# Kernel optimization log

Measured on AMD Instinct MI355X. Metric: run time of the kernel, lower is better.

## Reference

```python
import jax, jax.numpy as jnp
import numpy as np

B, H, N = 2, 4, 8192
K = 32       # sub_size
TEMP = 2.0   # temperature for the soft permutation indicator


def setup_inputs() -> dict:
    key = jax.random.key(0)
    ranking = jax.random.normal(key, (B, H, N, 1), dtype=jnp.float32)
    return {"ranking": ranking, "i": 0, "j": N}


@jax.custom_vjp
def hsigmoid(x):
    # Hard step indicator (x > 0) with straight-through gradient (CoCN Hsigmoid)
    return (x > 0).astype(x.dtype)

def _hs_fwd(x):
    return hsigmoid(x), None

def _hs_bwd(res, g):
    return (g,)

hsigmoid.defvjp(_hs_fwd, _hs_bwd)


def _windows(x, n, k):
    # circular pad last dim by k-1, then unfold into sliding windows of size k
    xp = jnp.concatenate([x, x[..., :k - 1]], axis=-1)
    idx = jnp.arange(n)[:, None] + jnp.arange(k)[None, :]   # (n, k)
    return xp[..., idx]                                      # (..., n, k)


def reference(ranking, i, j):
    b, h, n = ranking.shape[:3]
    k = K
    r = ranking[..., 0]                                      # (b,h,n)
    order = jnp.argsort(r, axis=2, stable=True)              # (b,h,n) stable sort indices
    r_sorted = jnp.take_along_axis(r, order, axis=2)

    val_win = _windows(r_sorted, n, k)                       # (b,h,n,k)
    idx_win = _windows(order.astype(jnp.float32), n, k).astype(jnp.int32)

    # scatter windows back to original node order == gather by inverse permutation
    inv = jnp.argsort(order, axis=2)                         # (b,h,n)
    val_win = jnp.take_along_axis(val_win, inv[..., None], axis=2)
    idx_win = jnp.take_along_axis(idx_win, inv[..., None], axis=2)

    # within each window, sort by original node index (stable), reorder values alike
    k_order = jnp.argsort(idx_win, axis=-1, stable=True)
    sorted_idx = jnp.take_along_axis(idx_win, k_order, axis=-1)
    val_win = jnp.take_along_axis(val_win, k_order, axis=-1)

    # slice node window [i, i+j)
    val_win = val_win[:, :, i:i + j]                         # (b,h,j,k)
    sorted_idx = sorted_idx[:, :, i:i + j]

    # (b,j,h,k) -> (b*j, h, k, 1)
    x = jnp.transpose(val_win, (0, 2, 1, 3)).reshape(-1, h, k, 1)
    rel = x - jnp.swapaxes(x, -1, -2)                        # (b*j,h,k,k)
    tie_bias = jnp.triu((rel == 0).astype(jnp.float32), 1)   # break ties above diagonal
    rel = rel + tie_bias
    uni = hsigmoid(jax.nn.relu(rel))                         # 1 where strictly greater
    rank = jnp.sum(uni, axis=-2, keepdims=True)              # (b*j,h,1,k)

    ind = jnp.arange(k, dtype=jnp.float32)[:, None] - rank   # (b*j,h,k,k)
    ind = jnp.where(ind < 0, ind + k, ind)
    perm = jnp.exp(-ind * TEMP)
    return perm, sorted_idx
```

## Files before the change

kernel.cpp:

```cpp
#include <hip/hip_runtime.h>
#include <stdint.h>

#define B_ 2
#define H_ 4
#define N_ 8192
#define K_ 32
#define ROWS 8
#define NTOT (ROWS * N_)
#define PERM_ELEMS ((size_t)B_ * N_ * H_ * K_ * K_)

__global__ __launch_bounds__(256) void pack_keys(const float* __restrict__ ranking,
                                                 uint64_t* __restrict__ keys) {
    const int g = blockIdx.x * 256 + threadIdx.x;
    uint32_t u = __float_as_uint(ranking[g]);
    u = (u & 0x80000000u) ? ~u : (u | 0x80000000u);
    keys[g] = ((uint64_t)u << 13) | (uint32_t)(g & (N_ - 1));
}

__global__ __launch_bounds__(256) void rank_scatter(const uint64_t* __restrict__ keys,
                                                    const float* __restrict__ ranking,
                                                    int2* __restrict__ vid,
                                                    int* __restrict__ inv) {
    __shared__ uint64_t jk[N_];
    const int row   = blockIdx.x >> 5;
    const int itile = blockIdx.x & 31;
    const uint64_t* rk = keys + (size_t)row * N_;

    for (int j = threadIdx.x; j < N_; j += 256)
        jk[j] = rk[j];

    const int i  = itile * 256 + threadIdx.x;
    const uint64_t my = rk[i];
    __syncthreads();

    int c0 = 0, c1 = 0, c2 = 0, c3 = 0;
    for (int j = 0; j < N_; j += 16) {
        uint64_t k[16];
        #pragma unroll
        for (int t = 0; t < 16; ++t) k[t] = jk[j + t];
        #pragma unroll
        for (int t = 0; t < 4; ++t) {
            c0 += (k[t * 4 + 0] < my);
            c1 += (k[t * 4 + 1] < my);
            c2 += (k[t * 4 + 2] < my);
            c3 += (k[t * 4 + 3] < my);
        }
    }
    const int s = c0 + c1 + c2 + c3;
    const int g = row * N_ + i;
    inv[g] = s;
    vid[(size_t)row * N_ + s] = make_int2(__float_as_int(ranking[g]), i);
}

__global__ __launch_bounds__(256) void windows_kernel(
    const int2* __restrict__ vid,
    const int* __restrict__ inv,
    float* __restrict__ perm_out,
    float* __restrict__ idx_out)
{
    __shared__ float etabP[K_];
    __shared__ uint64_t wk[8][K_];
    __shared__ float2 cinfo[8][K_ + 1];
    __shared__ float idf[8][K_];

    const int tid = threadIdx.x;
    if (tid < K_) etabP[tid] = expf(2.0f * (float)tid);

    const int wave = tid >> 6;
    const int lane = tid & 63;
    const int half = lane >> 5;
    const int m    = lane & 31;
    const int ws   = wave * 2 + half;

    const int w   = blockIdx.x * 8 + ws;
    const int row = w >> 13;
    const int n   = w & (N_ - 1);

    const int t = inv[(size_t)row * N_ + n];
    int g = t + m; if (g >= N_) g -= N_;
    const int2 vi = vid[(size_t)row * N_ + g];
    const int id = vi.y;
    uint32_t u = (uint32_t)vi.x;
    u = (u & 0x80000000u) ? ~u : (u | 0x80000000u);
    const int rid = (N_ - 1) - id;
    const uint64_t key2 = ((uint64_t)u << 13) | (uint32_t)rid;

    wk[ws][m] = key2;
    __syncthreads();

    int rank = 0, pos = 0;
    #pragma unroll
    for (int p = 0; p < K_; ++p) {
        const uint64_t kp = wk[ws][p];
        rank += (kp > key2);
        pos  += ((int)((uint32_t)kp & (uint32_t)(N_ - 1)) > rid);
    }

    cinfo[ws][pos] = make_float2(etabP[rank], __int_as_float(rank));
    idf[ws][pos]   = (float)id;
    __syncthreads();

    idx_out[((size_t)row * N_ + n) * K_ + m] = idf[ws][m];

    const int b = row >> 2;
    const int h = row & 3;
    float4* pout = (float4*)(perm_out + (((size_t)b * N_ + n) * H_ + h) * (K_ * K_));

    const int j0 = (m & 7) * 4;
    const float2 c0 = cinfo[ws][j0 + 0];
    const float2 c1 = cinfo[ws][j0 + 1];
    const float2 c2 = cinfo[ws][j0 + 2];
    const float2 c3 = cinfo[ws][j0 + 3];
    const int r0 = __float_as_int(c0.y), r1 = __float_as_int(c1.y);
    const int r2 = __float_as_int(c2.y), r3 = __float_as_int(c3.y);

    const int mbase = m >> 3;
    float a = (mbase & 1 ? 0.13533528f : 1.0f) * (mbase & 2 ? 0.018315639f : 1.0f);
    const float EM8 = 3.3546262e-4f;
    const float E64C = 1.6038108e-28f;
    int mm = mbase;

    #pragma unroll
    for (int q = 0; q < 8; ++q) {
        float4 val;
        val.x = a * c0.x * (mm < r0 ? E64C : 1.0f);
        val.y = a * c1.x * (mm < r1 ? E64C : 1.0f);
        val.z = a * c2.x * (mm < r2 ? E64C : 1.0f);
        val.w = a * c3.x * (mm < r3 ? E64C : 1.0f);
        pout[q * 32 + m] = val;
        a *= EM8;
        mm += 4;
    }
}

extern "C" void kernel_launch(void* const* d_in, const int* in_sizes, int n_in,
                              void* d_out, int out_size, void* d_ws, size_t ws_size,
                              hipStream_t stream) {
    const float* ranking = (const float*)d_in[0];

    char* ws = (char*)d_ws;
    uint64_t* keys = (uint64_t*)ws;
    int2*     vid  = (int2*)(ws + 512 * 1024);
    int*      inv  = (int*)(ws + 1024 * 1024);

    float* perm_out = (float*)d_out;
    float* idx_out  = perm_out + PERM_ELEMS;

    hipLaunchKernelGGL(pack_keys, dim3(NTOT / 256), dim3(256), 0, stream,
                       ranking, keys);
    hipLaunchKernelGGL(rank_scatter, dim3(256), dim3(256), 0, stream,
                       keys, ranking, vid, inv);
    hipLaunchKernelGGL(windows_kernel, dim3((ROWS * N_) / 8), dim3(256), 0, stream,
                       vid, inv, perm_out, idx_out);
}
```

Baseline: 333.6 us.

## Split rank counting into j-tiled partial counts with register-blocked keys

The rank-by-counting sort is restructured so each block compares 8 keys per thread against a 1024-key tile of the row, writing partial counts. A new scatter kernel sums the 8 partials to get each element's sorted position, then scatters values and indices. Each shared-memory key load is now reused across 8 comparisons, and LDS use per block shrinks, which raises occupancy. The cost is an extra kernel launch and a 2 MB partial-count buffer round trip through global memory.

```diff
diff --git a/kernel.cpp b/kernel.cpp
--- a/kernel.cpp
+++ b/kernel.cpp
@@ -17,39 +17,59 @@
     keys[g] = ((uint64_t)u << 13) | (uint32_t)(g & (N_ - 1));
 }
 
-__global__ __launch_bounds__(256) void rank_scatter(const uint64_t* __restrict__ keys,
-                                                    const float* __restrict__ ranking,
-                                                    int2* __restrict__ vid,
-                                                    int* __restrict__ inv) {
-    __shared__ uint64_t jk[N_];
-    const int row   = blockIdx.x >> 5;
-    const int itile = blockIdx.x & 31;
+#define JT 1024
+#define EPT 8
+
+__global__ __launch_bounds__(256) void rank_count(const uint64_t* __restrict__ keys,
+                                                  int* __restrict__ partial) {
+    __shared__ uint64_t jk[JT];
+    const int blk = blockIdx.x;
+    const int jt  = blk & 7;
+    const int it  = (blk >> 3) & 3;
+    const int row = blk >> 5;
     const uint64_t* rk = keys + (size_t)row * N_;
 
-    for (int j = threadIdx.x; j < N_; j += 256)
-        jk[j] = rk[j];
+    {
+        const ulonglong2* src = (const ulonglong2*)(rk + jt * JT);
+        ulonglong2* dst = (ulonglong2*)jk;
+        for (int j = threadIdx.x; j < JT / 2; j += 256) dst[j] = src[j];
+    }
 
-    const int i  = itile * 256 + threadIdx.x;
-    const uint64_t my = rk[i];
+    uint64_t my[EPT];
+    const int ibase = it * (EPT * 256) + threadIdx.x;
+    #pragma unroll
+    for (int e = 0; e < EPT; ++e) my[e] = rk[ibase + e * 256];
     __syncthreads();
 
-    int c0 = 0, c1 = 0, c2 = 0, c3 = 0;
-    for (int j = 0; j < N_; j += 16) {
-        uint64_t k[16];
+    int cnt[EPT] = {0, 0, 0, 0, 0, 0, 0, 0};
+    const ulonglong2* jv = (const ulonglong2*)jk;
+    for (int j = 0; j < JT / 2; j += 2) {
+        const ulonglong2 a = jv[j];
+        const ulonglong2 b = jv[j + 1];
         #pragma unroll
-        for (int t = 0; t < 16; ++t) k[t] = jk[j + t];
-        #pragma unroll
-        for (int t = 0; t < 4; ++t) {
-            c0 += (k[t * 4 + 0] < my);
-            c1 += (k[t * 4 + 1] < my);
-            c2 += (k[t * 4 + 2] < my);
-            c3 += (k[t * 4 + 3] < my);
+        for (int e = 0; e < EPT; ++e) {
+            cnt[e] += (a.x < my[e]);
+            cnt[e] += (a.y < my[e]);
+            cnt[e] += (b.x < my[e]);
+            cnt[e] += (b.y < my[e]);
         }
     }
-    const int s = c0 + c1 + c2 + c3;
-    const int g = row * N_ + i;
+    #pragma unroll
+    for (int e = 0; e < EPT; ++e)
+        partial[(size_t)jt * NTOT + (size_t)row * N_ + ibase + e * 256] = cnt[e];
+}
+
+__global__ __launch_bounds__(256) void scatter_sorted(const float* __restrict__ ranking,
+                                                      const int* __restrict__ partial,
+                                                      int2* __restrict__ vid,
+                                                      int* __restrict__ inv) {
+    const int g = blockIdx.x * 256 + threadIdx.x;
+    const int row = g >> 13;
+    int s = 0;
+    #pragma unroll
+    for (int jt = 0; jt < 8; ++jt) s += partial[(size_t)jt * NTOT + g];
     inv[g] = s;
-    vid[(size_t)row * N_ + s] = make_int2(__float_as_int(ranking[g]), i);
+    vid[(size_t)row * N_ + s] = make_int2(__float_as_int(ranking[g]), g & (N_ - 1));
 }
 
 __global__ __launch_bounds__(256) void windows_kernel(
@@ -139,17 +159,20 @@
     const float* ranking = (const float*)d_in[0];
 
     char* ws = (char*)d_ws;
-    uint64_t* keys = (uint64_t*)ws;
-    int2*     vid  = (int2*)(ws + 512 * 1024);
-    int*      inv  = (int*)(ws + 1024 * 1024);
+    uint64_t* keys    = (uint64_t*)ws;
+    int*      partial = (int*)(ws + 512 * 1024);
+    int2*     vid     = (int2*)(ws + 2560 * 1024);
+    int*      inv     = (int*)(ws + 3072 * 1024);
 
     float* perm_out = (float*)d_out;
     float* idx_out  = perm_out + PERM_ELEMS;
 
     hipLaunchKernelGGL(pack_keys, dim3(NTOT / 256), dim3(256), 0, stream,
                        ranking, keys);
-    hipLaunchKernelGGL(rank_scatter, dim3(256), dim3(256), 0, stream,
-                       keys, ranking, vid, inv);
+    hipLaunchKernelGGL(rank_count, dim3(256), dim3(256), 0, stream,
+                       keys, partial);
+    hipLaunchKernelGGL(scatter_sorted, dim3(NTOT / 256), dim3(256), 0, stream,
+                       ranking, partial, vid, inv);
     hipLaunchKernelGGL(windows_kernel, dim3((ROWS * N_) / 8), dim3(256), 0, stream,
                        vid, inv, perm_out, idx_out);
 }
```

After: 324.8 us. 2.6% less time.
